# Performance work log

Hardware: AMD Instinct MI355X
Metric: run time of the kernel (lower is better)

Reference implementation:

```python
import jax, jax.numpy as jnp
import numpy as np

EPS = 1e-8
LOSS_EPS = 1e-6
LOSS_WEIGHT = 1.0
N_BOXES = 262144

# ---------- rotated-2D-box helpers (mmcv diff_iou_rotated style) ----------

def box2corners_2d(box):
    # box: (N,5) = (x, y, w, h, alpha) -> corners (N,4,2), CCW order
    x, y, w, h, a = box[:, 0], box[:, 1], box[:, 2], box[:, 3], box[:, 4]
    x4 = jnp.array([0.5, -0.5, -0.5, 0.5], box.dtype) * w[:, None]   # (N,4)
    y4 = jnp.array([0.5, 0.5, -0.5, -0.5], box.dtype) * h[:, None]
    c, s = jnp.cos(a)[:, None], jnp.sin(a)[:, None]
    rx = x4 * c - y4 * s + x[:, None]
    ry = x4 * s + y4 * c + y[:, None]
    return jnp.stack([rx, ry], axis=-1)


def box_intersection(c1, c2):
    # segment-segment intersections between the 4 edges of each box
    # c1, c2: (N,4,2) -> pts (N,16,2), mask (N,16)
    l1 = jnp.concatenate([c1, jnp.roll(c1, -1, axis=1)], axis=-1)[:, :, None, :]  # (N,4,1,4)
    l2 = jnp.concatenate([c2, jnp.roll(c2, -1, axis=1)], axis=-1)[:, None, :, :]  # (N,1,4,4)
    x1, y1, x2, y2 = l1[..., 0], l1[..., 1], l1[..., 2], l1[..., 3]
    x3, y3, x4, y4 = l2[..., 0], l2[..., 1], l2[..., 2], l2[..., 3]
    num = (y4 - y3) * (x2 - x1) - (x4 - x3) * (y2 - y1)
    den_t = (x4 - x3) * (y1 - y3) - (y4 - y3) * (x1 - x3)
    den_u = (x2 - x1) * (y1 - y3) - (y2 - y1) * (x1 - x3)
    safe = jnp.where(num == 0.0, 1.0, num)
    t = jnp.where(num == 0.0, -1.0, den_t / safe)
    u = jnp.where(num == 0.0, -1.0, -den_u / safe)
    mask = (t > 0.0) & (t < 1.0) & (u > 0.0) & (u < 1.0)  # (N,4,4)
    t2 = den_t / (num + EPS)
    pts = jnp.stack([x1 + t2 * (x2 - x1), y1 + t2 * (y2 - y1)], axis=-1)
    pts = pts * mask[..., None]
    n = c1.shape[0]
    return pts.reshape(n, 16, 2), mask.reshape(n, 16)


def box_in_box(c1, c2):
    # which corners of box1 lie inside box2; c1,c2: (N,4,2) -> (N,4) bool
    a, b, d = c2[:, 0:1], c2[:, 1:2], c2[:, 3:4]
    ab, ad, am = b - a, d - a, c1 - a
    p_ab = jnp.sum(ab * am, -1) / jnp.sum(ab * ab, -1)
    p_ad = jnp.sum(ad * am, -1) / jnp.sum(ad * ad, -1)
    tol = 1e-6
    return (p_ab > -tol) & (p_ab < 1 + tol) & (p_ad > -tol) & (p_ad < 1 + tol)


def polygon_area(vertices, mask):
    # sort valid vertices CCW around their mean, close polygon, shoelace area
    # vertices: (N,24,2), mask: (N,24) bool -> area (N,)
    maskf = mask.astype(vertices.dtype)
    nv = jnp.maximum(jnp.sum(maskf, axis=1, keepdims=True), 1.0)
    mean = jnp.sum(vertices * maskf[..., None], axis=1, keepdims=True) / nv[..., None]
    v = vertices - mean
    ang = jnp.arctan2(v[..., 1], v[..., 0])
    # invalid vertices get huge, index-increasing keys so they sort last (stable)
    ang = jnp.where(mask, ang, 1e6 + jnp.arange(24, dtype=vertices.dtype))
    order = jnp.argsort(ang, axis=1)                         # (N,24) int
    vs = jnp.take_along_axis(v, order[..., None], axis=1)    # (N,24,2)
    ms = jnp.take_along_axis(mask, order, axis=1)
    first = vs[:, 0:1]                                       # first (valid) vertex
    vs = jnp.where(ms[..., None], vs, first)                 # pad closes polygon
    x, y = vs[..., 0], vs[..., 1]
    xn, yn = jnp.roll(x, -1, axis=1), jnp.roll(y, -1, axis=1)
    return 0.5 * jnp.abs(jnp.sum(x * yn - y * xn, axis=1))


def diff_iou_rotated_3d(b1, b2):
    # b1, b2: (N,7) = (x,y,z,w,h,l,alpha) -> IoU3D (N,)
    c1 = box2corners_2d(b1[:, jnp.array([0, 1, 3, 4, 6])])
    c2 = box2corners_2d(b2[:, jnp.array([0, 1, 3, 4, 6])])
    ipts, imask = box_intersection(c1, c2)
    m12 = box_in_box(c1, c2)
    m21 = box_in_box(c2, c1)
    vertices = jnp.concatenate([c1, c2, ipts], axis=1)   # (N,24,2)
    mask = jnp.concatenate([m12, m21, imask], axis=1)    # (N,24)
    inter_2d = polygon_area(vertices, mask)
    zmax1, zmin1 = b1[:, 2] + 0.5 * b1[:, 5], b1[:, 2] - 0.5 * b1[:, 5]
    zmax2, zmin2 = b2[:, 2] + 0.5 * b2[:, 5], b2[:, 2] - 0.5 * b2[:, 5]
    z_ov = jnp.maximum(jnp.minimum(zmax1, zmax2) - jnp.maximum(zmin1, zmin2), 0.0)
    inter_3d = inter_2d * z_ov
    vol1 = b1[:, 3] * b1[:, 4] * b1[:, 5]
    vol2 = b2[:, 3] * b2[:, 4] * b2[:, 5]
    return inter_3d / (vol1 + vol2 - inter_3d)


def corners_from_bboxes3d(b):
    # (N,7) -> (N,8,3); rotation about axis=1 (mmdet3d rotation_3d_in_axis)
    corners_norm = jnp.array([[-0.5, -0.5, -0.5], [-0.5, -0.5, 0.5],
                              [-0.5, 0.5, 0.5], [-0.5, 0.5, -0.5],
                              [0.5, -0.5, -0.5], [0.5, -0.5, 0.5],
                              [0.5, 0.5, 0.5], [0.5, 0.5, -0.5]], b.dtype)
    corners = corners_norm[None] * b[:, None, 3:6]          # (N,8,3)
    c, s = jnp.cos(b[:, 6])[:, None], jnp.sin(b[:, 6])[:, None]
    x, y, z = corners[..., 0], corners[..., 1], corners[..., 2]
    xr = x * c + z * s
    zr = -x * s + z * c
    return jnp.stack([xr, y, zr], axis=-1) + b[:, None, :3]


def diou_3d_loss(pred, target):
    iou3d = jnp.nan_to_num(diff_iou_rotated_3d(pred, target), nan=0.0)
    ctd = jnp.sum((pred[:, :3] - target[:, :3]) ** 2, axis=-1)
    cnd = jnp.mean(jnp.sum((corners_from_bboxes3d(pred)
                            - corners_from_bboxes3d(target)) ** 2, axis=-1), axis=1)
    did = jnp.sum(target[:, 3:6] ** 2, axis=-1)
    return 1.0 - iou3d + (ctd + cnd) / (ctd + cnd + did + LOSS_EPS)


def setup_inputs() -> dict:
    key = jax.random.key(0)
    k1, k2, k3, k4, k5 = jax.random.split(key, 5)
    xy = jax.random.uniform(k1, (N_BOXES, 2), minval=-40.0, maxval=40.0)
    z = jax.random.uniform(k2, (N_BOXES, 1), minval=-3.0, maxval=1.0)
    dims = jax.random.uniform(k3, (N_BOXES, 3), minval=0.8, maxval=4.0)
    ang = jax.random.uniform(k4, (N_BOXES, 1), minval=-np.pi, maxval=np.pi)
    target = jnp.concatenate([xy, z, dims, ang], axis=1).astype(jnp.float32)
    noise = jax.random.normal(k5, (N_BOXES, 7), jnp.float32) * \
        jnp.array([0.3, 0.3, 0.1, 0.2, 0.2, 0.2, 0.1], jnp.float32)
    pred = target + noise
    pred = pred.at[:, 3:6].set(jnp.maximum(pred[:, 3:6], 0.1))
    return {"pred": pred, "target": target}


def reference(pred, target):
    # DIOU3DLoss.forward with weight=None, reduction='mean'
    return LOSS_WEIGHT * jnp.mean(diou_3d_loss(pred, target))
```

## Files before the change

### kernel.cpp

```cpp
#include <hip/hip_runtime.h>
#include <math.h>

#define EPSI 1e-8f
#define TOLI 1e-6f

__device__ __forceinline__ float frcp(float x) { return __builtin_amdgcn_rcpf(x); }

#define CE(A, B) {                                  \
    unsigned ka = key[A], kb = key[B];              \
    key[A] = ka < kb ? ka : kb;                     \
    key[B] = ka < kb ? kb : ka; }

__global__ __launch_bounds__(64) void diou3d_main(
    const float* __restrict__ pred, const float* __restrict__ tgt,
    float* __restrict__ partial, int n)
{
    __shared__ float2 vbuf[24][64];
    int lane = threadIdx.x;
    int tid = blockIdx.x * 64 + lane;
    float loss = 0.0f;
    if (tid < n) {
        const float* P = pred + (size_t)tid * 7;
        const float* T = tgt  + (size_t)tid * 7;
        float p0 = P[0], p1 = P[1], p2 = P[2], p3 = P[3], p4 = P[4], p5 = P[5], p6 = P[6];
        float t0 = T[0], t1 = T[1], t2 = T[2], t3 = T[3], t4 = T[4], t5 = T[5], t6 = T[6];

        float sp, cp, st, ct;
        __sincosf(p6, &sp, &cp);
        __sincosf(t6, &st, &ct);
        const float hx[4] = {0.5f, -0.5f, -0.5f, 0.5f};
        const float hy[4] = {0.5f, 0.5f, -0.5f, -0.5f};
        float c1x[4], c1y[4], c2x[4], c2y[4];
#pragma unroll
        for (int k = 0; k < 4; k++) {
            float xa = hx[k] * p3, ya = hy[k] * p4;
            c1x[k] = xa * cp - ya * sp + p0;
            c1y[k] = xa * sp + ya * cp + p1;
            float xb = hx[k] * t3, yb = hy[k] * t4;
            c2x[k] = xb * ct - yb * st + t0;
            c2y[k] = xb * st + yb * ct + t1;
        }

        float vx[24], vy[24];
        bool  vm[24];

        {
            float abx = c2x[1] - c2x[0], aby = c2y[1] - c2y[0];
            float adx = c2x[3] - c2x[0], ady = c2y[3] - c2y[0];
            float rab = frcp(abx * abx + aby * aby);
            float rad = frcp(adx * adx + ady * ady);
#pragma unroll
            for (int k = 0; k < 4; k++) {
                float amx = c1x[k] - c2x[0], amy = c1y[k] - c2y[0];
                float pab = (abx * amx + aby * amy) * rab;
                float pad = (adx * amx + ady * amy) * rad;
                vm[k] = (pab > -TOLI) && (pab < 1.0f + TOLI) && (pad > -TOLI) && (pad < 1.0f + TOLI);
                vx[k] = c1x[k]; vy[k] = c1y[k];
            }
        }
        {
            float abx = c1x[1] - c1x[0], aby = c1y[1] - c1y[0];
            float adx = c1x[3] - c1x[0], ady = c1y[3] - c1y[0];
            float rab = frcp(abx * abx + aby * aby);
            float rad = frcp(adx * adx + ady * ady);
#pragma unroll
            for (int k = 0; k < 4; k++) {
                float amx = c2x[k] - c1x[0], amy = c2y[k] - c1y[0];
                float pab = (abx * amx + aby * amy) * rab;
                float pad = (adx * amx + ady * amy) * rad;
                vm[4 + k] = (pab > -TOLI) && (pab < 1.0f + TOLI) && (pad > -TOLI) && (pad < 1.0f + TOLI);
                vx[4 + k] = c2x[k]; vy[4 + k] = c2y[k];
            }
        }

#pragma unroll
        for (int i = 0; i < 4; i++) {
            float x1 = c1x[i], y1 = c1y[i];
            float dx12 = c1x[(i + 1) & 3] - x1, dy12 = c1y[(i + 1) & 3] - y1;
#pragma unroll
            for (int j = 0; j < 4; j++) {
                float x3 = c2x[j], y3 = c2y[j];
                float dx34 = c2x[(j + 1) & 3] - x3, dy34 = c2y[(j + 1) & 3] - y3;
                float num  = dy34 * dx12 - dx34 * dy12;
                float dxs = x1 - x3, dys = y1 - y3;
                float den_t = dx34 * dys - dy34 * dxs;
                float den_u = dx12 * dys - dy12 * dxs;
                bool m = (den_t * num > 0.0f) && ((num - den_t) * num > 0.0f)
                      && (den_u * num < 0.0f) && ((num + den_u) * num > 0.0f);
                float t2d = den_t * frcp(num + EPSI);
                int idx = 8 + i * 4 + j;
                vx[idx] = x1 + t2d * dx12;
                vy[idx] = y1 + t2d * dy12;
                vm[idx] = m;
            }
        }

        float cntf = 0.0f, sx = 0.0f, sy = 0.0f;
#pragma unroll
        for (int k = 0; k < 24; k++) {
            cntf += vm[k] ? 1.0f : 0.0f;
            sx   += vm[k] ? vx[k] : 0.0f;
            sy   += vm[k] ? vy[k] : 0.0f;
        }
        int ic = (int)cntf;
        float rnv = frcp(fmaxf(cntf, 1.0f));
        float mx = sx * rnv, my = sy * rnv;

        unsigned key[24];
#pragma unroll
        for (int k = 0; k < 24; k++) {
            float ux = vx[k] - mx, uy = vy[k] - my;
            vbuf[k][lane] = make_float2(ux, uy);
            float d = fabsf(ux) + fabsf(uy);
            float pq = ux * frcp(d);
            pq = (d == 0.0f) ? 0.0f : pq;
            float ang = (uy < 0.0f) ? (pq - 1.0f) : (1.0f - pq);
            unsigned u = __float_as_uint(ang);
            u ^= (unsigned)(((int)u >> 31)) | 0x80000000u;
            unsigned kk = (u & 0xFFFFFFE0u) | (unsigned)k;
            key[k] = vm[k] ? kk : (0xFFFFFFE0u | (unsigned)k);
        }

#pragma unroll
        for (int p = 1; p < 32; p <<= 1) {
#pragma unroll
            for (int k = p; k >= 1; k >>= 1) {
#pragma unroll
                for (int j = k & (p - 1); j + k < 32; j += 2 * k) {
#pragma unroll
                    for (int i = 0; i < k; i++) {
                        int lo = i + j, hi = i + j + k;
                        if (hi < 24 && (lo / (2 * p) == hi / (2 * p))) {
                            CE(lo, hi);
                        }
                    }
                }
            }
        }

        float gx[12], gy[12];
#pragma unroll
        for (int s = 0; s < 12; s++) {
            int idx = (int)(key[s] & 31u);
            float2 v = vbuf[idx][lane];
            gx[s] = v.x; gy[s] = v.y;
        }

        float x0 = gx[0], y0 = gy[0];
#pragma unroll
        for (int s = 0; s < 12; s++) {
            bool v = (s < ic);
            gx[s] = v ? gx[s] : x0;
            gy[s] = v ? gy[s] : y0;
        }
        float area2 = 0.0f;
#pragma unroll
        for (int s = 0; s < 12; s++) {
            int ns = (s == 11) ? 0 : s + 1;
            area2 += gx[s] * gy[ns] - gy[s] * gx[ns];
        }
        float inter2d = 0.5f * fabsf(area2);

        float zmax1 = p2 + 0.5f * p5, zmin1 = p2 - 0.5f * p5;
        float zmax2 = t2 + 0.5f * t5, zmin2 = t2 - 0.5f * t5;
        float zov = fmaxf(fminf(zmax1, zmax2) - fmaxf(zmin1, zmin2), 0.0f);
        float inter3d = inter2d * zov;
        float vol1 = p3 * p4 * p5, vol2 = t3 * t4 * t5;
        float iou = inter3d / (vol1 + vol2 - inter3d);
        if (isnan(iou)) iou = 0.0f;

        float d0 = p0 - t0, d1 = p1 - t1, d2 = p2 - t2;
        float ctd = d0 * d0 + d1 * d1 + d2 * d2;

        float cosd = cp * ct + sp * st;
        float dp2 = p3 * p3 + p4 * p4 + p5 * p5;
        float dt2 = t3 * t3 + t4 * t4 + t5 * t5;
        float crossd = p3 * t3 * cosd + p4 * t4 + p5 * t5 * cosd;
        float cnd = ctd + 0.25f * (dp2 + dt2) - 0.5f * crossd;

        float dterm = (ctd + cnd) / (ctd + cnd + dt2 + 1e-6f);
        loss = 1.0f - iou + dterm;
    }

#pragma unroll
    for (int off = 32; off > 0; off >>= 1) loss += __shfl_down(loss, off);
    if (threadIdx.x == 0) partial[blockIdx.x] = loss;
}

__global__ __launch_bounds__(256) void diou3d_reduce(
    const float* __restrict__ partial, int nblocks, float* __restrict__ out, float invn)
{
    float s = 0.0f;
    for (int i = threadIdx.x; i < nblocks; i += 256) s += partial[i];
#pragma unroll
    for (int off = 32; off > 0; off >>= 1) s += __shfl_down(s, off);
    __shared__ float wsum[4];
    int lane = threadIdx.x & 63, wid = threadIdx.x >> 6;
    if (lane == 0) wsum[wid] = s;
    __syncthreads();
    if (threadIdx.x == 0)
        out[0] = (wsum[0] + wsum[1] + wsum[2] + wsum[3]) * invn;
}

extern "C" void kernel_launch(void* const* d_in, const int* in_sizes, int n_in,
                              void* d_out, int out_size, void* d_ws, size_t ws_size,
                              hipStream_t stream) {
    const float* pred = (const float*)d_in[0];
    const float* tgt  = (const float*)d_in[1];
    float* out = (float*)d_out;
    int n = in_sizes[0] / 7;
    const int T = 64;
    int blocks = (n + T - 1) / T;
    float* partial = (float*)d_ws;
    diou3d_main<<<blocks, T, 0, stream>>>(pred, tgt, partial, n);
    diou3d_reduce<<<1, 256, 0, stream>>>(partial, blocks, out, 1.0f / (float)n);
}
```

Measured before the change: 81.22 us.

## Process two boxes per thread and store sort vertices as packed fp16 in LDS

Each thread now computes the loss for two boxes, with the per-box work moved into an inline helper, and the grid is halved. Centred polygon vertices are stored in shared memory as packed half2 through cvt_pkrtz instead of float2, which halves LDS footprint and traffic per vertex. The launch bounds gain a minimum of 2 waves per EU, and tail threads clamp their index rather than branch. The aims are more instruction-level parallelism and less per-block overhead, at the cost of fp16 rounding in the shoelace area (an accuracy risk for boxes far from the centroid) and possible register pressure.

```diff
diff --git a/kernel.cpp b/kernel.cpp
--- a/kernel.cpp
+++ b/kernel.cpp
@@ -3,6 +3,8 @@
 
 #define EPSI 1e-8f
 #define TOLI 1e-6f
+
+typedef __fp16 half2v __attribute__((ext_vector_type(2)));
 
 __device__ __forceinline__ float frcp(float x) { return __builtin_amdgcn_rcpf(x); }
 
@@ -11,180 +13,192 @@
     key[A] = ka < kb ? ka : kb;                     \
     key[B] = ka < kb ? kb : ka; }
 
-__global__ __launch_bounds__(64) void diou3d_main(
+__device__ __forceinline__ float box_loss(
+    const float* __restrict__ P, const float* __restrict__ T,
+    unsigned (*__restrict__ vb)[64], int lane)
+{
+    float p0 = P[0], p1 = P[1], p2 = P[2], p3 = P[3], p4 = P[4], p5 = P[5], p6 = P[6];
+    float t0 = T[0], t1 = T[1], t2 = T[2], t3 = T[3], t4 = T[4], t5 = T[5], t6 = T[6];
+
+    float sp, cp, st, ct;
+    __sincosf(p6, &sp, &cp);
+    __sincosf(t6, &st, &ct);
+    const float hx[4] = {0.5f, -0.5f, -0.5f, 0.5f};
+    const float hy[4] = {0.5f, 0.5f, -0.5f, -0.5f};
+    float c1x[4], c1y[4], c2x[4], c2y[4];
+#pragma unroll
+    for (int k = 0; k < 4; k++) {
+        float xa = hx[k] * p3, ya = hy[k] * p4;
+        c1x[k] = xa * cp - ya * sp + p0;
+        c1y[k] = xa * sp + ya * cp + p1;
+        float xb = hx[k] * t3, yb = hy[k] * t4;
+        c2x[k] = xb * ct - yb * st + t0;
+        c2y[k] = xb * st + yb * ct + t1;
+    }
+
+    float vx[24], vy[24];
+    bool  vm[24];
+
+    {
+        float abx = c2x[1] - c2x[0], aby = c2y[1] - c2y[0];
+        float adx = c2x[3] - c2x[0], ady = c2y[3] - c2y[0];
+        float rab = frcp(abx * abx + aby * aby);
+        float rad = frcp(adx * adx + ady * ady);
+#pragma unroll
+        for (int k = 0; k < 4; k++) {
+            float amx = c1x[k] - c2x[0], amy = c1y[k] - c2y[0];
+            float pab = (abx * amx + aby * amy) * rab;
+            float pad = (adx * amx + ady * amy) * rad;
+            vm[k] = (pab > -TOLI) && (pab < 1.0f + TOLI) && (pad > -TOLI) && (pad < 1.0f + TOLI);
+            vx[k] = c1x[k]; vy[k] = c1y[k];
+        }
+    }
+    {
+        float abx = c1x[1] - c1x[0], aby = c1y[1] - c1y[0];
+        float adx = c1x[3] - c1x[0], ady = c1y[3] - c1y[0];
+        float rab = frcp(abx * abx + aby * aby);
+        float rad = frcp(adx * adx + ady * ady);
+#pragma unroll
+        for (int k = 0; k < 4; k++) {
+            float amx = c2x[k] - c1x[0], amy = c2y[k] - c1y[0];
+            float pab = (abx * amx + aby * amy) * rab;
+            float pad = (adx * amx + ady * amy) * rad;
+            vm[4 + k] = (pab > -TOLI) && (pab < 1.0f + TOLI) && (pad > -TOLI) && (pad < 1.0f + TOLI);
+            vx[4 + k] = c2x[k]; vy[4 + k] = c2y[k];
+        }
+    }
+
+#pragma unroll
+    for (int i = 0; i < 4; i++) {
+        float x1 = c1x[i], y1 = c1y[i];
+        float dx12 = c1x[(i + 1) & 3] - x1, dy12 = c1y[(i + 1) & 3] - y1;
+#pragma unroll
+        for (int j = 0; j < 4; j++) {
+            float x3 = c2x[j], y3 = c2y[j];
+            float dx34 = c2x[(j + 1) & 3] - x3, dy34 = c2y[(j + 1) & 3] - y3;
+            float num  = dy34 * dx12 - dx34 * dy12;
+            float dxs = x1 - x3, dys = y1 - y3;
+            float den_t = dx34 * dys - dy34 * dxs;
+            float den_u = dx12 * dys - dy12 * dxs;
+            bool m = (den_t * num > 0.0f) && ((num - den_t) * num > 0.0f)
+                  && (den_u * num < 0.0f) && ((num + den_u) * num > 0.0f);
+            float t2d = den_t * frcp(num + EPSI);
+            int idx = 8 + i * 4 + j;
+            vx[idx] = x1 + t2d * dx12;
+            vy[idx] = y1 + t2d * dy12;
+            vm[idx] = m;
+        }
+    }
+
+    float cntf = 0.0f, sx = 0.0f, sy = 0.0f;
+#pragma unroll
+    for (int k = 0; k < 24; k++) {
+        cntf += vm[k] ? 1.0f : 0.0f;
+        sx   += vm[k] ? vx[k] : 0.0f;
+        sy   += vm[k] ? vy[k] : 0.0f;
+    }
+    int ic = (int)cntf;
+    float rnv = frcp(fmaxf(cntf, 1.0f));
+    float mx = sx * rnv, my = sy * rnv;
+
+    unsigned key[24];
+#pragma unroll
+    for (int k = 0; k < 24; k++) {
+        float ux = vx[k] - mx, uy = vy[k] - my;
+        half2v h = __builtin_amdgcn_cvt_pkrtz(ux, uy);
+        vb[k][lane] = __builtin_bit_cast(unsigned, h);
+        float d = fabsf(ux) + fabsf(uy);
+        float pq = ux * frcp(d);
+        pq = (d == 0.0f) ? 0.0f : pq;
+        float ang = (uy < 0.0f) ? (pq - 1.0f) : (1.0f - pq);
+        unsigned u = __float_as_uint(ang);
+        u ^= (unsigned)(((int)u >> 31)) | 0x80000000u;
+        unsigned kk = (u & 0xFFFFFFE0u) | (unsigned)k;
+        key[k] = vm[k] ? kk : (0xFFFFFFE0u | (unsigned)k);
+    }
+
+#pragma unroll
+    for (int p = 1; p < 32; p <<= 1) {
+#pragma unroll
+        for (int k = p; k >= 1; k >>= 1) {
+#pragma unroll
+            for (int j = k & (p - 1); j + k < 32; j += 2 * k) {
+#pragma unroll
+                for (int i = 0; i < k; i++) {
+                    int lo = i + j, hi = i + j + k;
+                    if (hi < 24 && (lo / (2 * p) == hi / (2 * p))) {
+                        CE(lo, hi);
+                    }
+                }
+            }
+        }
+    }
+
+    float gx[12], gy[12];
+#pragma unroll
+    for (int s = 0; s < 12; s++) {
+        int idx = (int)(key[s] & 31u);
+        half2v h = __builtin_bit_cast(half2v, vb[idx][lane]);
+        gx[s] = (float)h.x; gy[s] = (float)h.y;
+    }
+
+    float x0 = gx[0], y0 = gy[0];
+#pragma unroll
+    for (int s = 0; s < 12; s++) {
+        bool v = (s < ic);
+        gx[s] = v ? gx[s] : x0;
+        gy[s] = v ? gy[s] : y0;
+    }
+    float area2 = 0.0f;
+#pragma unroll
+    for (int s = 0; s < 12; s++) {
+        int ns = (s == 11) ? 0 : s + 1;
+        area2 += gx[s] * gy[ns] - gy[s] * gx[ns];
+    }
+    float inter2d = 0.5f * fabsf(area2);
+
+    float zmax1 = p2 + 0.5f * p5, zmin1 = p2 - 0.5f * p5;
+    float zmax2 = t2 + 0.5f * t5, zmin2 = t2 - 0.5f * t5;
+    float zov = fmaxf(fminf(zmax1, zmax2) - fmaxf(zmin1, zmin2), 0.0f);
+    float inter3d = inter2d * zov;
+    float vol1 = p3 * p4 * p5, vol2 = t3 * t4 * t5;
+    float iou = inter3d / (vol1 + vol2 - inter3d);
+    if (isnan(iou)) iou = 0.0f;
+
+    float d0 = p0 - t0, d1 = p1 - t1, d2 = p2 - t2;
+    float ctd = d0 * d0 + d1 * d1 + d2 * d2;
+
+    float cosd = cp * ct + sp * st;
+    float dp2 = p3 * p3 + p4 * p4 + p5 * p5;
+    float dt2 = t3 * t3 + t4 * t4 + t5 * t5;
+    float crossd = p3 * t3 * cosd + p4 * t4 + p5 * t5 * cosd;
+    float cnd = ctd + 0.25f * (dp2 + dt2) - 0.5f * crossd;
+
+    float dterm = (ctd + cnd) / (ctd + cnd + dt2 + 1e-6f);
+    return 1.0f - iou + dterm;
+}
+
+__global__ __launch_bounds__(64, 2) void diou3d_main(
     const float* __restrict__ pred, const float* __restrict__ tgt,
     float* __restrict__ partial, int n)
 {
-    __shared__ float2 vbuf[24][64];
+    __shared__ unsigned vbuf[48][64];
     int lane = threadIdx.x;
-    int tid = blockIdx.x * 64 + lane;
-    float loss = 0.0f;
-    if (tid < n) {
-        const float* P = pred + (size_t)tid * 7;
-        const float* T = tgt  + (size_t)tid * 7;
-        float p0 = P[0], p1 = P[1], p2 = P[2], p3 = P[3], p4 = P[4], p5 = P[5], p6 = P[6];
-        float t0 = T[0], t1 = T[1], t2 = T[2], t3 = T[3], t4 = T[4], t5 = T[5], t6 = T[6];
-
-        float sp, cp, st, ct;
-        __sincosf(p6, &sp, &cp);
-        __sincosf(t6, &st, &ct);
-        const float hx[4] = {0.5f, -0.5f, -0.5f, 0.5f};
-        const float hy[4] = {0.5f, 0.5f, -0.5f, -0.5f};
-        float c1x[4], c1y[4], c2x[4], c2y[4];
-#pragma unroll
-        for (int k = 0; k < 4; k++) {
-            float xa = hx[k] * p3, ya = hy[k] * p4;
-            c1x[k] = xa * cp - ya * sp + p0;
-            c1y[k] = xa * sp + ya * cp + p1;
-            float xb = hx[k] * t3, yb = hy[k] * t4;
-            c2x[k] = xb * ct - yb * st + t0;
-            c2y[k] = xb * st + yb * ct + t1;
-        }
-
-        float vx[24], vy[24];
-        bool  vm[24];
-
-        {
-            float abx = c2x[1] - c2x[0], aby = c2y[1] - c2y[0];
-            float adx = c2x[3] - c2x[0], ady = c2y[3] - c2y[0];
-            float rab = frcp(abx * abx + aby * aby);
-            float rad = frcp(adx * adx + ady * ady);
-#pragma unroll
-            for (int k = 0; k < 4; k++) {
-                float amx = c1x[k] - c2x[0], amy = c1y[k] - c2y[0];
-                float pab = (abx * amx + aby * amy) * rab;
-                float pad = (adx * amx + ady * amy) * rad;
-                vm[k] = (pab > -TOLI) && (pab < 1.0f + TOLI) && (pad > -TOLI) && (pad < 1.0f + TOLI);
-                vx[k] = c1x[k]; vy[k] = c1y[k];
-            }
-        }
-        {
-            float abx = c1x[1] - c1x[0], aby = c1y[1] - c1y[0];
-            float adx = c1x[3] - c1x[0], ady = c1y[3] - c1y[0];
-            float rab = frcp(abx * abx + aby * aby);
-            float rad = frcp(adx * adx + ady * ady);
-#pragma unroll
-            for (int k = 0; k < 4; k++) {
-                float amx = c2x[k] - c1x[0], amy = c2y[k] - c1y[0];
-                float pab = (abx * amx + aby * amy) * rab;
-                float pad = (adx * amx + ady * amy) * rad;
-                vm[4 + k] = (pab > -TOLI) && (pab < 1.0f + TOLI) && (pad > -TOLI) && (pad < 1.0f + TOLI);
-                vx[4 + k] = c2x[k]; vy[4 + k] = c2y[k];
-            }
-        }
-
-#pragma unroll
-        for (int i = 0; i < 4; i++) {
-            float x1 = c1x[i], y1 = c1y[i];
-            float dx12 = c1x[(i + 1) & 3] - x1, dy12 = c1y[(i + 1) & 3] - y1;
-#pragma unroll
-            for (int j = 0; j < 4; j++) {
-                float x3 = c2x[j], y3 = c2y[j];
-                float dx34 = c2x[(j + 1) & 3] - x3, dy34 = c2y[(j + 1) & 3] - y3;
-                float num  = dy34 * dx12 - dx34 * dy12;
-                float dxs = x1 - x3, dys = y1 - y3;
-                float den_t = dx34 * dys - dy34 * dxs;
-                float den_u = dx12 * dys - dy12 * dxs;
-                bool m = (den_t * num > 0.0f) && ((num - den_t) * num > 0.0f)
-                      && (den_u * num < 0.0f) && ((num + den_u) * num > 0.0f);
-                float t2d = den_t * frcp(num + EPSI);
-                int idx = 8 + i * 4 + j;
-                vx[idx] = x1 + t2d * dx12;
-                vy[idx] = y1 + t2d * dy12;
-                vm[idx] = m;
-            }
-        }
-
-        float cntf = 0.0f, sx = 0.0f, sy = 0.0f;
-#pragma unroll
-        for (int k = 0; k < 24; k++) {
-            cntf += vm[k] ? 1.0f : 0.0f;
-            sx   += vm[k] ? vx[k] : 0.0f;
-            sy   += vm[k] ? vy[k] : 0.0f;
-        }
-        int ic = (int)cntf;
-        float rnv = frcp(fmaxf(cntf, 1.0f));
-        float mx = sx * rnv, my = sy * rnv;
-
-        unsigned key[24];
-#pragma unroll
-        for (int k = 0; k < 24; k++) {
-            float ux = vx[k] - mx, uy = vy[k] - my;
-            vbuf[k][lane] = make_float2(ux, uy);
-            float d = fabsf(ux) + fabsf(uy);
-            float pq = ux * frcp(d);
-            pq = (d == 0.0f) ? 0.0f : pq;
-            float ang = (uy < 0.0f) ? (pq - 1.0f) : (1.0f - pq);
-            unsigned u = __float_as_uint(ang);
-            u ^= (unsigned)(((int)u >> 31)) | 0x80000000u;
-            unsigned kk = (u & 0xFFFFFFE0u) | (unsigned)k;
-            key[k] = vm[k] ? kk : (0xFFFFFFE0u | (unsigned)k);
-        }
-
-#pragma unroll
-        for (int p = 1; p < 32; p <<= 1) {
-#pragma unroll
-            for (int k = p; k >= 1; k >>= 1) {
-#pragma unroll
-                for (int j = k & (p - 1); j + k < 32; j += 2 * k) {
-#pragma unroll
-                    for (int i = 0; i < k; i++) {
-                        int lo = i + j, hi = i + j + k;
-                        if (hi < 24 && (lo / (2 * p) == hi / (2 * p))) {
-                            CE(lo, hi);
-                        }
-                    }
-                }
-            }
-        }
-
-        float gx[12], gy[12];
-#pragma unroll
-        for (int s = 0; s < 12; s++) {
-            int idx = (int)(key[s] & 31u);
-            float2 v = vbuf[idx][lane];
-            gx[s] = v.x; gy[s] = v.y;
-        }
-
-        float x0 = gx[0], y0 = gy[0];
-#pragma unroll
-        for (int s = 0; s < 12; s++) {
-            bool v = (s < ic);
-            gx[s] = v ? gx[s] : x0;
-            gy[s] = v ? gy[s] : y0;
-        }
-        float area2 = 0.0f;
-#pragma unroll
-        for (int s = 0; s < 12; s++) {
-            int ns = (s == 11) ? 0 : s + 1;
-            area2 += gx[s] * gy[ns] - gy[s] * gx[ns];
-        }
-        float inter2d = 0.5f * fabsf(area2);
-
-        float zmax1 = p2 + 0.5f * p5, zmin1 = p2 - 0.5f * p5;
-        float zmax2 = t2 + 0.5f * t5, zmin2 = t2 - 0.5f * t5;
-        float zov = fmaxf(fminf(zmax1, zmax2) - fmaxf(zmin1, zmin2), 0.0f);
-        float inter3d = inter2d * zov;
-        float vol1 = p3 * p4 * p5, vol2 = t3 * t4 * t5;
-        float iou = inter3d / (vol1 + vol2 - inter3d);
-        if (isnan(iou)) iou = 0.0f;
-
-        float d0 = p0 - t0, d1 = p1 - t1, d2 = p2 - t2;
-        float ctd = d0 * d0 + d1 * d1 + d2 * d2;
-
-        float cosd = cp * ct + sp * st;
-        float dp2 = p3 * p3 + p4 * p4 + p5 * p5;
-        float dt2 = t3 * t3 + t4 * t4 + t5 * t5;
-        float crossd = p3 * t3 * cosd + p4 * t4 + p5 * t5 * cosd;
-        float cnd = ctd + 0.25f * (dp2 + dt2) - 0.5f * crossd;
-
-        float dterm = (ctd + cnd) / (ctd + cnd + dt2 + 1e-6f);
-        loss = 1.0f - iou + dterm;
-    }
-
-#pragma unroll
-    for (int off = 32; off > 0; off >>= 1) loss += __shfl_down(loss, off);
-    if (threadIdx.x == 0) partial[blockIdx.x] = loss;
+    int base = blockIdx.x * 128;
+    float losses = 0.0f;
+#pragma unroll
+    for (int b = 0; b < 2; b++) {
+        int tid = base + b * 64 + lane;
+        int ctid = tid < n ? tid : (n - 1);
+        float keep = (tid < n) ? 1.0f : 0.0f;
+        unsigned (*vb)[64] = &vbuf[b * 24];
+        float l = box_loss(pred + (size_t)ctid * 7, tgt + (size_t)ctid * 7, vb, lane);
+        losses += keep * l;
+    }
+
+#pragma unroll
+    for (int off = 32; off > 0; off >>= 1) losses += __shfl_down(losses, off);
+    if (lane == 0) partial[blockIdx.x] = losses;
 }
 
 __global__ __launch_bounds__(256) void diou3d_reduce(
@@ -209,9 +223,8 @@
     const float* tgt  = (const float*)d_in[1];
     float* out = (float*)d_out;
     int n = in_sizes[0] / 7;
-    const int T = 64;
-    int blocks = (n + T - 1) / T;
+    int blocks = (n + 127) / 128;
     float* partial = (float*)d_ws;
-    diou3d_main<<<blocks, T, 0, stream>>>(pred, tgt, partial, n);
+    diou3d_main<<<blocks, 64, 0, stream>>>(pred, tgt, partial, n);
     diou3d_reduce<<<1, 256, 0, stream>>>(partial, blocks, out, 1.0f / (float)n);
 }
```

Measured after the change: 77.13 us. -5.0%, faster.
